# Kernel optimization log

Measured on AMD Instinct MI355X. Metric: run time of the kernel, lower is better.

## Reference

```python
import jax, jax.numpy as jnp
import numpy as np

H = 2  # num_heads hardcoded in the torch module


def setup_inputs() -> dict:
    key = jax.random.key(0)
    ks = jax.random.split(key, 10)
    B, S, D = 8, 2048, 512
    s = 0.02
    return {
        "rgb": jax.random.normal(ks[0], (B, S, D), jnp.float32),
        "event": jax.random.normal(ks[1], (B, S, D), jnp.float32),
        "w_rgb": jax.random.normal(ks[2], (D, D), jnp.float32) * s,
        "b_rgb": jnp.zeros((D,), jnp.float32),
        "w_event": jax.random.normal(ks[3], (D, D), jnp.float32) * s,
        "b_event": jnp.zeros((D,), jnp.float32),
        "w_in": jax.random.normal(ks[4], (3 * D, D), jnp.float32) * s,   # packed QKV in_proj, torch layout
        "b_in": jnp.zeros((3 * D,), jnp.float32),
        "w_out": jax.random.normal(ks[5], (D, D), jnp.float32) * s,
        "b_out": jnp.zeros((D,), jnp.float32),
    }


def _mha(q_in, kv_in, w_in, b_in, w_out, b_out):
    """torch nn.MultiheadAttention with key==value==kv_in, batch-first math."""
    B, S, D = q_in.shape
    hd = D // H
    q = q_in @ w_in[:D].T + b_in[:D]
    k = kv_in @ w_in[D:2 * D].T + b_in[D:2 * D]
    v = kv_in @ w_in[2 * D:].T + b_in[2 * D:]
    q = q.reshape(B, S, H, hd) * (1.0 / np.sqrt(hd))
    k = k.reshape(B, S, H, hd)
    v = v.reshape(B, S, H, hd)
    scores = jnp.einsum('bqhd,bkhd->bhqk', q, k)          # [B,H,S,S]
    attn = jax.nn.softmax(scores, axis=-1)
    out = jnp.einsum('bhqk,bkhd->bqhd', attn, v).reshape(B, S, D)
    return out @ w_out.T + b_out


def reference(rgb, event, w_rgb, b_rgb, w_event, b_event, w_in, b_in, w_out, b_out):
    rgb_p = rgb @ w_rgb.T + b_rgb
    event_p = event @ w_event.T + b_event
    # same attention weights used for both cross directions
    event_attn = _mha(rgb_p, event_p, w_in, b_in, w_out, b_out)
    rgb_attn = _mha(event_p, rgb_p, w_in, b_in, w_out, b_out)
    gate = jax.nn.sigmoid(jnp.sum(rgb_p * event_p, axis=-1, keepdims=True))
    fused = gate * event_attn + (1.0 - gate) * rgb_attn
    return fused + (rgb_p + event_p) * 0.5
```

## Files before the change

kernel.cpp:

```cpp
#include <hip/hip_runtime.h>
#include <hip/hip_bf16.h>
#include <stdint.h>


typedef __bf16 bf16_t;
typedef __bf16 bf16x8 __attribute__((ext_vector_type(8)));
typedef float f32x4 __attribute__((ext_vector_type(4)));
typedef float f32x16 __attribute__((ext_vector_type(16)));
typedef unsigned int u32;

typedef void gvoid_t __attribute__((address_space(1)));
typedef void svoid_t __attribute__((address_space(3)));

__device__ inline void gload16(const void* g, void* l) {
    __builtin_amdgcn_global_load_lds((gvoid_t*)g, (svoid_t*)l, 16, 0, 0);
}

__device__ inline u32 cvtpk_bf16(float lo, float hi) {
    u32 r;
    asm("v_cvt_pk_bf16_f32 %0, %1, %2" : "=v"(r) : "v"(lo), "v"(hi));
    return r;
}

__global__ __launch_bounds__(256) void f2b_kernel(const float* __restrict__ in,
                                                  bf16_t* __restrict__ out, int n8) {
    int i = blockIdx.x * 256 + threadIdx.x;
    if (i >= n8) return;
    const float4* p = reinterpret_cast<const float4*>(in) + (size_t)i * 2;
    float4 a = p[0], b = p[1];
    bf16x8 o;
    o[0] = (bf16_t)a.x; o[1] = (bf16_t)a.y; o[2] = (bf16_t)a.z; o[3] = (bf16_t)a.w;
    o[4] = (bf16_t)b.x; o[5] = (bf16_t)b.y; o[6] = (bf16_t)b.z; o[7] = (bf16_t)b.w;
    reinterpret_cast<bf16x8*>(out)[i] = o;
}

template <int MODE>
__global__ __launch_bounds__(256) void gemm_bt(const bf16_t* __restrict__ A,
                                               const bf16_t* __restrict__ Bw,
                                               const float* __restrict__ bias,
                                               void* __restrict__ Cout,
                                               const bf16_t* __restrict__ r1,
                                               const bf16_t* __restrict__ r2,
                                               bf16_t* __restrict__ qdst,
                                               bf16_t* __restrict__ kdst,
                                               bf16_t* __restrict__ vdst,
                                               int M, int N, int K) {
    __shared__ __align__(16) bf16_t As[128][64];
    __shared__ __align__(16) bf16_t Bs[128][64];
    const int tid = threadIdx.x, lane = tid & 63, w = tid >> 6;
    const int l16 = lane & 15, l4 = lane >> 4;
    const int wm = w >> 1, wn = w & 1;
    const size_t a0 = (size_t)blockIdx.y * 128;
    const size_t b0 = (size_t)blockIdx.x * 128;
    f32x4 acc[4][4] = {};
    const int srow = w * 32 + (lane >> 3);
    const int scol = (lane & 7) * 8;
    for (int kt = 0; kt < K; kt += 64) {
        __syncthreads();
#pragma unroll
        for (int i = 0; i < 4; ++i) {
            gload16(A + (a0 + srow + i * 8) * (size_t)K + kt + scol, &As[w * 32 + i * 8][0]);
            gload16(Bw + (b0 + srow + i * 8) * (size_t)K + kt + scol, &Bs[w * 32 + i * 8][0]);
        }
        __syncthreads();
#pragma unroll
        for (int kk = 0; kk < 2; ++kk) {
            bf16x8 af[4], bfr[4];
#pragma unroll
            for (int mi = 0; mi < 4; ++mi)
                af[mi] = *reinterpret_cast<const bf16x8*>(&As[wm * 64 + mi * 16 + l16][kk * 32 + l4 * 8]);
#pragma unroll
            for (int ni = 0; ni < 4; ++ni)
                bfr[ni] = *reinterpret_cast<const bf16x8*>(&Bs[wn * 64 + ni * 16 + l16][kk * 32 + l4 * 8]);
#pragma unroll
            for (int mi = 0; mi < 4; ++mi)
#pragma unroll
                for (int ni = 0; ni < 4; ++ni)
                    acc[mi][ni] = __builtin_amdgcn_mfma_f32_16x16x32_bf16(af[mi], bfr[ni], acc[mi][ni], 0, 0, 0);
        }
    }
#pragma unroll
    for (int mi = 0; mi < 4; ++mi) {
#pragma unroll
        for (int ni = 0; ni < 4; ++ni) {
            int col = (int)b0 + wn * 64 + ni * 16 + l16;
            float bs = bias[col];
            int row0 = (int)a0 + wm * 64 + mi * 16 + l4 * 4;
            float vv[4];
#pragma unroll
            for (int r = 0; r < 4; ++r) vv[r] = acc[mi][ni][r] + bs;
            if (MODE == 0) {
#pragma unroll
                for (int r = 0; r < 4; ++r)
                    ((bf16_t*)Cout)[(size_t)(row0 + r) * N + col] = (bf16_t)vv[r];
            } else if (MODE == 2) {
#pragma unroll
                for (int r = 0; r < 4; ++r) {
                    size_t idx = (size_t)(row0 + r) * N + col;
                    ((float*)Cout)[idx] = vv[r] + 0.5f * ((float)r1[idx] + (float)r2[idx]);
                }
            } else {
                if (col < 512) {
#pragma unroll
                    for (int r = 0; r < 4; ++r)
                        qdst[(size_t)(row0 + r) * 512 + col] = (bf16_t)(vv[r] * 0.0625f);
                } else if (col < 1024) {
                    int cc = col - 512, h = cc >> 8, d = cc & 255;
#pragma unroll
                    for (int r = 0; r < 4; ++r) {
                        int row = row0 + r;
                        int bh = (row >> 11) * 2 + h, seq = row & 2047;
                        kdst[((size_t)(bh * 64 + (seq >> 5))) * 8192 + (d >> 3) * 256 +
                             (seq & 31) * 8 + (d & 7)] = (bf16_t)vv[r];
                    }
                } else {
                    int cc = col - 1024, h = cc >> 8, d = cc & 255;
                    int bh = (row0 >> 11) * 2 + h, seq = row0 & 2047;
                    size_t idx = ((size_t)(bh * 64 + (seq >> 5))) * 8192 +
                                 ((seq >> 3) & 3) * 2048 + d * 8 + (seq & 7);
                    union { bf16_t h4[4]; uint2 u8; } pk;
#pragma unroll
                    for (int r = 0; r < 4; ++r) pk.h4[r] = (bf16_t)vv[r];
                    *reinterpret_cast<uint2*>(&vdst[idx]) = pk.u8;
                }
            }
        }
    }
}

__global__ __launch_bounds__(256) void gate_kernel(const bf16_t* __restrict__ rp,
                                                   const bf16_t* __restrict__ ep,
                                                   float* __restrict__ gate) {
    int row = blockIdx.x * 4 + (threadIdx.x >> 6);
    int lane = threadIdx.x & 63;
    bf16x8 a = reinterpret_cast<const bf16x8*>(rp + (size_t)row * 512)[lane];
    bf16x8 b = reinterpret_cast<const bf16x8*>(ep + (size_t)row * 512)[lane];
    float s = 0.f;
#pragma unroll
    for (int j = 0; j < 8; ++j) s += (float)a[j] * (float)b[j];
#pragma unroll
    for (int off = 32; off; off >>= 1) s += __shfl_xor(s, off, 64);
    if (lane == 0) gate[row] = 1.f / (1.f + __expf(-s));
}

__global__ __launch_bounds__(256, 2) void attn_kernel(const bf16_t* __restrict__ qbr,
                                                      const bf16_t* __restrict__ qbe,
                                                      const bf16_t* __restrict__ kbr,
                                                      const bf16_t* __restrict__ kbe,
                                                      const bf16_t* __restrict__ vbr,
                                                      const bf16_t* __restrict__ vbe,
                                                      bf16_t* __restrict__ out0,
                                                      bf16_t* __restrict__ out1) {
    __shared__ __align__(16) bf16_t smem[32768];
    const int bid = blockIdx.x;
    const int qb = bid >> 5;
    const int combo = bid & 31;
    const int dir = combo >> 4;
    const int bh = combo & 15;
    const int b = bh >> 1, h = bh & 1;
    const bf16_t* Qb = dir ? qbe : qbr;
    const bf16_t* Kc = dir ? kbr : kbe;
    const bf16_t* Vc = dir ? vbr : vbe;
    bf16_t* osrc = dir ? out1 : out0;
    const int tid = threadIdx.x;
    const int w = tid >> 6, l = tid & 63;
    const int l31 = l & 31, hi = l >> 5;
    const int q0w = qb * 128 + w * 32;

    const bf16_t* qp = Qb + ((size_t)(b * 2048 + q0w + l31)) * 512 + h * 256 + hi * 8;
    bf16x8 qf[16];
#pragma unroll
    for (int dch = 0; dch < 16; ++dch)
        qf[dch] = *reinterpret_cast<const bf16x8*>(qp + dch * 16);

    f32x16 O[8] = {};
    float mrun = -1e30f, lrun = 0.f;

    const bf16_t* kq = Kc + (size_t)bh * 524288 + (w * 2048 + l * 8);
    const bf16_t* vq = Vc + (size_t)bh * 524288 + (w * 2048 + l * 8);

#define STAGE(t, nb)                                              \
    do {                                                          \
        const bf16_t* ks_ = kq + (size_t)(t) * 8192;              \
        const bf16_t* vs_ = vq + (size_t)(t) * 8192;              \
        bf16_t* lk_ = &smem[(nb) * 16384 + w * 2048];             \
        bf16_t* lv_ = &smem[(nb) * 16384 + 8192 + w * 2048];      \
        gload16(ks_, lk_);                                        \
        gload16(ks_ + 512, lk_ + 512);                            \
        gload16(ks_ + 1024, lk_ + 1024);                          \
        gload16(ks_ + 1536, lk_ + 1536);                          \
        gload16(vs_, lv_);                                        \
        gload16(vs_ + 512, lv_ + 512);                            \
        gload16(vs_ + 1024, lv_ + 1024);                          \
        gload16(vs_ + 1536, lv_ + 1536);                          \
    } while (0)

    STAGE(0, 0);

    for (int kt2 = 0; kt2 < 64; ++kt2) {
        asm volatile("s_waitcnt vmcnt(0)" ::: "memory");
        __builtin_amdgcn_s_barrier();
        asm volatile("" ::: "memory");
        if (kt2 < 63) STAGE(kt2 + 1, (kt2 + 1) & 1);
        asm volatile("" ::: "memory");

        const int cb = kt2 & 1;
        const bf16_t* kb = &smem[cb * 16384 + hi * 256 + l31 * 8];
        const bf16_t* vb = &smem[cb * 16384 + 8192 + hi * 2048 + l31 * 8];

        f32x16 st = {};
#pragma unroll
        for (int dch = 0; dch < 16; ++dch) {
            bf16x8 kf = *reinterpret_cast<const bf16x8*>(kb + dch * 512);
            st = __builtin_amdgcn_mfma_f32_32x32x16_bf16(kf, qf[dch], st, 0, 0, 0);
        }

        float mx = -1e30f;
#pragma unroll
        for (int r = 0; r < 16; ++r) mx = fmaxf(mx, st[r]);
        mx = fmaxf(mx, __shfl_xor(mx, 32, 64));
        if (__any(mx - mrun > 8.f)) {
            float mnew = fmaxf(mrun, mx);
            float sc = __expf(mrun - mnew);
            mrun = mnew;
            lrun *= sc;
#pragma unroll
            for (int r = 0; r < 16; ++r) {
                int qr = (r & 3) + 8 * (r >> 2) + 4 * hi;
                float scr = __shfl(sc, qr, 64);
#pragma unroll
                for (int g = 0; g < 8; ++g) O[g][r] *= scr;
            }
        }
        float lsum = 0.f;
        u32 W[8];
#pragma unroll
        for (int m = 0; m < 8; ++m) {
            float plo = __expf(st[2 * m] - mrun);
            float phi_ = __expf(st[2 * m + 1] - mrun);
            lsum += plo + phi_;
            W[m] = cvtpk_bf16(plo, phi_);
        }
        lsum += __shfl_xor(lsum, 32, 64);
        lrun += lsum;

#pragma unroll
        for (int s = 0; s < 2; ++s) {
            u32 t0 = hi ? W[4 * s] : W[4 * s + 2];
            u32 t1 = hi ? W[4 * s + 1] : W[4 * s + 3];
            u32 r0 = (u32)__shfl_xor((int)t0, 32, 64);
            u32 r1 = (u32)__shfl_xor((int)t1, 32, 64);
            union { u32 uw[4]; bf16x8 v; } a;
            a.uw[0] = hi ? r0 : W[4 * s];
            a.uw[1] = hi ? r1 : W[4 * s + 1];
            a.uw[2] = hi ? W[4 * s + 2] : r0;
            a.uw[3] = hi ? W[4 * s + 3] : r1;
#pragma unroll
            for (int g = 0; g < 8; ++g) {
                bf16x8 vf = *reinterpret_cast<const bf16x8*>(vb + s * 4096 + g * 256);
                O[g] = __builtin_amdgcn_mfma_f32_32x32x16_bf16(a.v, vf, O[g], 0, 0, 0);
            }
        }
    }
#undef STAGE

#pragma unroll
    for (int r = 0; r < 16; ++r) {
        int qr = (r & 3) + 8 * (r >> 2) + 4 * hi;
        float linv = 1.0f / __shfl(lrun, qr, 64);
        size_t rowoff = ((size_t)(b * 2048 + q0w + qr)) * 512 + h * 256 + l31;
#pragma unroll
        for (int g = 0; g < 8; ++g)
            osrc[rowoff + g * 32] = (bf16_t)(O[g][r] * linv);
    }
}

__global__ __launch_bounds__(256) void mix_kernel(const bf16_t* __restrict__ a1,
                                                  const bf16_t* __restrict__ a2,
                                                  const float* __restrict__ gate,
                                                  bf16_t* __restrict__ outm) {
    int i = blockIdx.x * 256 + threadIdx.x;
    int m = i >> 6;
    float g = gate[m];
    bf16x8 x = reinterpret_cast<const bf16x8*>(a1)[i];
    bf16x8 y = reinterpret_cast<const bf16x8*>(a2)[i];
    bf16x8 o;
#pragma unroll
    for (int j = 0; j < 8; ++j) o[j] = (bf16_t)(g * (float)x[j] + (1.f - g) * (float)y[j]);
    reinterpret_cast<bf16x8*>(outm)[i] = o;
}

extern "C" void kernel_launch(void* const* d_in, const int* in_sizes, int n_in,
                              void* d_out, int out_size, void* d_ws, size_t ws_size,
                              hipStream_t stream) {
    const float* rgb = (const float*)d_in[0];
    const float* event = (const float*)d_in[1];
    const float* w_rgb = (const float*)d_in[2];
    const float* b_rgb = (const float*)d_in[3];
    const float* w_event = (const float*)d_in[4];
    const float* b_event = (const float*)d_in[5];
    const float* w_in = (const float*)d_in[6];
    const float* b_in = (const float*)d_in[7];
    const float* w_out = (const float*)d_in[8];
    const float* b_out = (const float*)d_in[9];
    float* out = (float*)d_out;

    const int M = 16384;
    const size_t MB16 = (size_t)16 * 1024 * 1024;
    char* ws = (char*)d_ws;
    bf16_t* wrgb_bf = (bf16_t*)(ws + 0);
    bf16_t* wevt_bf = (bf16_t*)(ws + 524288);
    bf16_t* wout_bf = (bf16_t*)(ws + 1048576);
    bf16_t* win_bf = (bf16_t*)(ws + 1572864);
    float* gate = (float*)(ws + 3145728);
    bf16_t* bufA = (bf16_t*)(ws + 4194304);
    bf16_t* bufB = (bf16_t*)(ws + 4194304 + MB16);
    bf16_t* rgbp = (bf16_t*)(ws + 4194304 + 2 * MB16);
    bf16_t* evtp = (bf16_t*)(ws + 4194304 + 3 * MB16);
    bf16_t* qbr  = (bf16_t*)(ws + 4194304 + 4 * MB16);
    bf16_t* qbe  = (bf16_t*)(ws + 4194304 + 5 * MB16);
    bf16_t* kbr  = (bf16_t*)(ws + 4194304 + 6 * MB16);
    bf16_t* kbe  = (bf16_t*)(ws + 4194304 + 7 * MB16);
    bf16_t* vbr  = (bf16_t*)(ws + 4194304 + 8 * MB16);
    bf16_t* vbe  = (bf16_t*)(ws + 4194304 + 9 * MB16);
    bf16_t* mixed = (bf16_t*)(ws + 4194304 + 10 * MB16);

    dim3 blk(256);
    f2b_kernel<<<4096, blk, 0, stream>>>(rgb, bufA, M * 512 / 8);
    f2b_kernel<<<4096, blk, 0, stream>>>(event, bufB, M * 512 / 8);
    f2b_kernel<<<128, blk, 0, stream>>>(w_rgb, wrgb_bf, 512 * 512 / 8);
    f2b_kernel<<<128, blk, 0, stream>>>(w_event, wevt_bf, 512 * 512 / 8);
    f2b_kernel<<<384, blk, 0, stream>>>(w_in, win_bf, 1536 * 512 / 8);
    f2b_kernel<<<128, blk, 0, stream>>>(w_out, wout_bf, 512 * 512 / 8);
    gemm_bt<0><<<dim3(4, 128), blk, 0, stream>>>(bufA, wrgb_bf, b_rgb, rgbp, nullptr, nullptr,
                                                 nullptr, nullptr, nullptr, M, 512, 512);
    gemm_bt<0><<<dim3(4, 128), blk, 0, stream>>>(bufB, wevt_bf, b_event, evtp, nullptr, nullptr,
                                                 nullptr, nullptr, nullptr, M, 512, 512);
    gate_kernel<<<4096, blk, 0, stream>>>(rgbp, evtp, gate);
    gemm_bt<1><<<dim3(12, 128), blk, 0, stream>>>(rgbp, win_bf, b_in, nullptr, nullptr, nullptr,
                                                  qbr, kbr, vbr, M, 1536, 512);
    gemm_bt<1><<<dim3(12, 128), blk, 0, stream>>>(evtp, win_bf, b_in, nullptr, nullptr, nullptr,
                                                  qbe, kbe, vbe, M, 1536, 512);
    attn_kernel<<<512, blk, 0, stream>>>(qbr, qbe, kbr, kbe, vbr, vbe, bufA, bufB);
    mix_kernel<<<4096, blk, 0, stream>>>(bufA, bufB, gate, mixed);
    gemm_bt<2><<<dim3(4, 128), blk, 0, stream>>>(mixed, wout_bf, b_out, out, rgbp, evtp,
                                                 nullptr, nullptr, nullptr, M, 512, 512);
}
```

Baseline: 374.1 us.

## Batch launches, fuse gate-mix into out-proj GEMM, use exp2 softmax with setprio

Merges the six fp32-to-bf16 conversions into one kernel and batches the paired rgb/event projection GEMMs into single launches via a doubled grid. The gate mix is folded into the A-tile load of the output GEMM, so the separate mix kernel and its intermediate buffer go away. In attention it folds log2(e) into the Q scale so softmax can use raw v_exp_f32, adds s_setprio around the MFMA sections, and splits the PV loop. The intent is to cut launch overhead and memory round-trips. The cost is that the out-proj GEMM now loads A through registers instead of direct-to-LDS loads.

```diff
diff --git a/kernel.cpp b/kernel.cpp
--- a/kernel.cpp
+++ b/kernel.cpp
@@ -22,46 +22,94 @@
     return r;
 }
 
-__global__ __launch_bounds__(256) void f2b_kernel(const float* __restrict__ in,
-                                                  bf16_t* __restrict__ out, int n8) {
+__device__ inline float exp2v(float x) {
+    float r;
+    asm("v_exp_f32 %0, %1" : "=v"(r) : "v"(x));
+    return r;
+}
+
+__global__ __launch_bounds__(256) void f2b_all(const float* __restrict__ s0, bf16_t* __restrict__ d0,
+                                               const float* __restrict__ s1, bf16_t* __restrict__ d1,
+                                               const float* __restrict__ s2, bf16_t* __restrict__ d2,
+                                               const float* __restrict__ s3, bf16_t* __restrict__ d3,
+                                               const float* __restrict__ s4, bf16_t* __restrict__ d4,
+                                               const float* __restrict__ s5, bf16_t* __restrict__ d5) {
     int i = blockIdx.x * 256 + threadIdx.x;
-    if (i >= n8) return;
-    const float4* p = reinterpret_cast<const float4*>(in) + (size_t)i * 2;
+    const float* s; bf16_t* d; int off;
+    if (i < 1048576)      { s = s0; d = d0; off = i; }
+    else if (i < 2097152) { s = s1; d = d1; off = i - 1048576; }
+    else if (i < 2129920) { s = s2; d = d2; off = i - 2097152; }
+    else if (i < 2162688) { s = s3; d = d3; off = i - 2129920; }
+    else if (i < 2260992) { s = s4; d = d4; off = i - 2162688; }
+    else                  { s = s5; d = d5; off = i - 2260992; }
+    const float4* p = reinterpret_cast<const float4*>(s) + (size_t)off * 2;
     float4 a = p[0], b = p[1];
     bf16x8 o;
     o[0] = (bf16_t)a.x; o[1] = (bf16_t)a.y; o[2] = (bf16_t)a.z; o[3] = (bf16_t)a.w;
     o[4] = (bf16_t)b.x; o[5] = (bf16_t)b.y; o[6] = (bf16_t)b.z; o[7] = (bf16_t)b.w;
-    reinterpret_cast<bf16x8*>(out)[i] = o;
+    reinterpret_cast<bf16x8*>(d)[off] = o;
 }
 
 template <int MODE>
 __global__ __launch_bounds__(256) void gemm_bt(const bf16_t* __restrict__ A,
+                                               const bf16_t* __restrict__ A2,
                                                const bf16_t* __restrict__ Bw,
+                                               const bf16_t* __restrict__ Bw2,
                                                const float* __restrict__ bias,
+                                               const float* __restrict__ bias2,
                                                void* __restrict__ Cout,
+                                               void* __restrict__ Cout2,
                                                const bf16_t* __restrict__ r1,
                                                const bf16_t* __restrict__ r2,
+                                               const float* __restrict__ gate,
                                                bf16_t* __restrict__ qdst,
                                                bf16_t* __restrict__ kdst,
                                                bf16_t* __restrict__ vdst,
-                                               int M, int N, int K) {
+                                               bf16_t* __restrict__ qdst2,
+                                               bf16_t* __restrict__ kdst2,
+                                               bf16_t* __restrict__ vdst2,
+                                               int N, int K) {
     __shared__ __align__(16) bf16_t As[128][64];
     __shared__ __align__(16) bf16_t Bs[128][64];
     const int tid = threadIdx.x, lane = tid & 63, w = tid >> 6;
     const int l16 = lane & 15, l4 = lane >> 4;
     const int wm = w >> 1, wn = w & 1;
-    const size_t a0 = (size_t)blockIdx.y * 128;
+    const bool sec = (MODE != 2) && (blockIdx.y >= 128);
+    const size_t a0 = (size_t)(blockIdx.y & 127) * 128;
     const size_t b0 = (size_t)blockIdx.x * 128;
+    const bf16_t* Ap = sec ? A2 : A;
+    const bf16_t* Bp = sec ? Bw2 : Bw;
+    const float* bp = sec ? bias2 : bias;
     f32x4 acc[4][4] = {};
     const int srow = w * 32 + (lane >> 3);
     const int scol = (lane & 7) * 8;
+    float g4[4];
+    if (MODE == 2) {
+#pragma unroll
+        for (int i = 0; i < 4; ++i) g4[i] = gate[a0 + srow + i * 8];
+    }
     for (int kt = 0; kt < K; kt += 64) {
         __syncthreads();
-#pragma unroll
-        for (int i = 0; i < 4; ++i) {
-            gload16(A + (a0 + srow + i * 8) * (size_t)K + kt + scol, &As[w * 32 + i * 8][0]);
-            gload16(Bw + (b0 + srow + i * 8) * (size_t)K + kt + scol, &Bs[w * 32 + i * 8][0]);
-        }
+        if (MODE == 2) {
+#pragma unroll
+            for (int i = 0; i < 4; ++i) {
+                size_t ro = (a0 + srow + i * 8) * (size_t)K + kt + scol;
+                bf16x8 x = *reinterpret_cast<const bf16x8*>(A + ro);
+                bf16x8 y = *reinterpret_cast<const bf16x8*>(A2 + ro);
+                bf16x8 o;
+#pragma unroll
+                for (int j = 0; j < 8; ++j)
+                    o[j] = (bf16_t)(g4[i] * (float)x[j] + (1.f - g4[i]) * (float)y[j]);
+                *reinterpret_cast<bf16x8*>(&As[srow + i * 8 - (lane >> 3) + (lane >> 3)][scol]) = o;
+            }
+        } else {
+#pragma unroll
+            for (int i = 0; i < 4; ++i)
+                gload16(Ap + (a0 + srow + i * 8) * (size_t)K + kt + scol, &As[w * 32 + i * 8][0]);
+        }
+#pragma unroll
+        for (int i = 0; i < 4; ++i)
+            gload16(Bp + (b0 + srow + i * 8) * (size_t)K + kt + scol, &Bs[w * 32 + i * 8][0]);
         __syncthreads();
 #pragma unroll
         for (int kk = 0; kk < 2; ++kk) {
@@ -79,20 +127,24 @@
                     acc[mi][ni] = __builtin_amdgcn_mfma_f32_16x16x32_bf16(af[mi], bfr[ni], acc[mi][ni], 0, 0, 0);
         }
     }
+    bf16_t* qd = sec ? qdst2 : qdst;
+    bf16_t* kd = sec ? kdst2 : kdst;
+    bf16_t* vd = sec ? vdst2 : vdst;
 #pragma unroll
     for (int mi = 0; mi < 4; ++mi) {
 #pragma unroll
         for (int ni = 0; ni < 4; ++ni) {
             int col = (int)b0 + wn * 64 + ni * 16 + l16;
-            float bs = bias[col];
+            float bs = bp[col];
             int row0 = (int)a0 + wm * 64 + mi * 16 + l4 * 4;
             float vv[4];
 #pragma unroll
             for (int r = 0; r < 4; ++r) vv[r] = acc[mi][ni][r] + bs;
             if (MODE == 0) {
+                bf16_t* Cp = (bf16_t*)(sec ? Cout2 : Cout);
 #pragma unroll
                 for (int r = 0; r < 4; ++r)
-                    ((bf16_t*)Cout)[(size_t)(row0 + r) * N + col] = (bf16_t)vv[r];
+                    Cp[(size_t)(row0 + r) * N + col] = (bf16_t)vv[r];
             } else if (MODE == 2) {
 #pragma unroll
                 for (int r = 0; r < 4; ++r) {
@@ -103,15 +155,15 @@
                 if (col < 512) {
 #pragma unroll
                     for (int r = 0; r < 4; ++r)
-                        qdst[(size_t)(row0 + r) * 512 + col] = (bf16_t)(vv[r] * 0.0625f);
+                        qd[(size_t)(row0 + r) * 512 + col] = (bf16_t)(vv[r] * 0.090168440f);
                 } else if (col < 1024) {
                     int cc = col - 512, h = cc >> 8, d = cc & 255;
 #pragma unroll
                     for (int r = 0; r < 4; ++r) {
                         int row = row0 + r;
                         int bh = (row >> 11) * 2 + h, seq = row & 2047;
-                        kdst[((size_t)(bh * 64 + (seq >> 5))) * 8192 + (d >> 3) * 256 +
-                             (seq & 31) * 8 + (d & 7)] = (bf16_t)vv[r];
+                        kd[((size_t)(bh * 64 + (seq >> 5))) * 8192 + (d >> 3) * 256 +
+                           (seq & 31) * 8 + (d & 7)] = (bf16_t)vv[r];
                     }
                 } else {
                     int cc = col - 1024, h = cc >> 8, d = cc & 255;
@@ -121,7 +173,7 @@
                     union { bf16_t h4[4]; uint2 u8; } pk;
 #pragma unroll
                     for (int r = 0; r < 4; ++r) pk.h4[r] = (bf16_t)vv[r];
-                    *reinterpret_cast<uint2*>(&vdst[idx]) = pk.u8;
+                    *reinterpret_cast<uint2*>(&vd[idx]) = pk.u8;
                 }
             }
         }
@@ -174,25 +226,23 @@
         qf[dch] = *reinterpret_cast<const bf16x8*>(qp + dch * 16);
 
     f32x16 O[8] = {};
+    f32x16 st;
     float mrun = -1e30f, lrun = 0.f;
+    union PA { u32 uw[4]; bf16x8 v; } pa0, pa1;
 
     const bf16_t* kq = Kc + (size_t)bh * 524288 + (w * 2048 + l * 8);
     const bf16_t* vq = Vc + (size_t)bh * 524288 + (w * 2048 + l * 8);
 
-#define STAGE(t, nb)                                              \
-    do {                                                          \
-        const bf16_t* ks_ = kq + (size_t)(t) * 8192;              \
-        const bf16_t* vs_ = vq + (size_t)(t) * 8192;              \
-        bf16_t* lk_ = &smem[(nb) * 16384 + w * 2048];             \
-        bf16_t* lv_ = &smem[(nb) * 16384 + 8192 + w * 2048];      \
-        gload16(ks_, lk_);                                        \
-        gload16(ks_ + 512, lk_ + 512);                            \
-        gload16(ks_ + 1024, lk_ + 1024);                          \
-        gload16(ks_ + 1536, lk_ + 1536);                          \
-        gload16(vs_, lv_);                                        \
-        gload16(vs_ + 512, lv_ + 512);                            \
-        gload16(vs_ + 1024, lv_ + 1024);                          \
-        gload16(vs_ + 1536, lv_ + 1536);                          \
+#define STAGE(T, P)                                                    \
+    do {                                                               \
+        const bf16_t* ks_ = kq + (size_t)(T) * 8192;                   \
+        const bf16_t* vs_ = vq + (size_t)(T) * 8192;                   \
+        bf16_t* lk_ = &smem[(P) * 8192 + w * 2048];                    \
+        bf16_t* lv_ = &smem[16384 + (P) * 8192 + w * 2048];            \
+        gload16(ks_, lk_); gload16(ks_ + 512, lk_ + 512);              \
+        gload16(ks_ + 1024, lk_ + 1024); gload16(ks_ + 1536, lk_ + 1536); \
+        gload16(vs_, lv_); gload16(vs_ + 512, lv_ + 512);              \
+        gload16(vs_ + 1024, lv_ + 1024); gload16(vs_ + 1536, lv_ + 1536); \
     } while (0)
 
     STAGE(0, 0);
@@ -200,28 +250,29 @@
     for (int kt2 = 0; kt2 < 64; ++kt2) {
         asm volatile("s_waitcnt vmcnt(0)" ::: "memory");
         __builtin_amdgcn_s_barrier();
-        asm volatile("" ::: "memory");
         if (kt2 < 63) STAGE(kt2 + 1, (kt2 + 1) & 1);
-        asm volatile("" ::: "memory");
 
         const int cb = kt2 & 1;
-        const bf16_t* kb = &smem[cb * 16384 + hi * 256 + l31 * 8];
-        const bf16_t* vb = &smem[cb * 16384 + 8192 + hi * 2048 + l31 * 8];
-
-        f32x16 st = {};
+        const bf16_t* kb = &smem[cb * 8192 + hi * 256 + l31 * 8];
+        const bf16_t* vb = &smem[16384 + cb * 8192 + hi * 2048 + l31 * 8];
+
+#pragma unroll
+        for (int r = 0; r < 16; ++r) st[r] = 0.f;
+        __builtin_amdgcn_s_setprio(1);
 #pragma unroll
         for (int dch = 0; dch < 16; ++dch) {
             bf16x8 kf = *reinterpret_cast<const bf16x8*>(kb + dch * 512);
             st = __builtin_amdgcn_mfma_f32_32x32x16_bf16(kf, qf[dch], st, 0, 0, 0);
         }
-
-        float mx = -1e30f;
-#pragma unroll
-        for (int r = 0; r < 16; ++r) mx = fmaxf(mx, st[r]);
+        __builtin_amdgcn_s_setprio(0);
+
+        float mx = st[0];
+#pragma unroll
+        for (int r = 1; r < 16; ++r) mx = fmaxf(mx, st[r]);
         mx = fmaxf(mx, __shfl_xor(mx, 32, 64));
         if (__any(mx - mrun > 8.f)) {
             float mnew = fmaxf(mrun, mx);
-            float sc = __expf(mrun - mnew);
+            float sc = exp2v(mrun - mnew);
             mrun = mnew;
             lrun *= sc;
 #pragma unroll
@@ -236,31 +287,40 @@
         u32 W[8];
 #pragma unroll
         for (int m = 0; m < 8; ++m) {
-            float plo = __expf(st[2 * m] - mrun);
-            float phi_ = __expf(st[2 * m + 1] - mrun);
+            float plo = exp2v(st[2 * m] - mrun);
+            float phi_ = exp2v(st[2 * m + 1] - mrun);
             lsum += plo + phi_;
             W[m] = cvtpk_bf16(plo, phi_);
         }
         lsum += __shfl_xor(lsum, 32, 64);
         lrun += lsum;
-
-#pragma unroll
-        for (int s = 0; s < 2; ++s) {
-            u32 t0 = hi ? W[4 * s] : W[4 * s + 2];
-            u32 t1 = hi ? W[4 * s + 1] : W[4 * s + 3];
+        {
+            u32 t0 = hi ? W[0] : W[2], t1 = hi ? W[1] : W[3];
             u32 r0 = (u32)__shfl_xor((int)t0, 32, 64);
             u32 r1 = (u32)__shfl_xor((int)t1, 32, 64);
-            union { u32 uw[4]; bf16x8 v; } a;
-            a.uw[0] = hi ? r0 : W[4 * s];
-            a.uw[1] = hi ? r1 : W[4 * s + 1];
-            a.uw[2] = hi ? W[4 * s + 2] : r0;
-            a.uw[3] = hi ? W[4 * s + 3] : r1;
-#pragma unroll
-            for (int g = 0; g < 8; ++g) {
-                bf16x8 vf = *reinterpret_cast<const bf16x8*>(vb + s * 4096 + g * 256);
-                O[g] = __builtin_amdgcn_mfma_f32_32x32x16_bf16(a.v, vf, O[g], 0, 0, 0);
-            }
-        }
+            pa0.uw[0] = hi ? r0 : W[0]; pa0.uw[1] = hi ? r1 : W[1];
+            pa0.uw[2] = hi ? W[2] : r0; pa0.uw[3] = hi ? W[3] : r1;
+        }
+        {
+            u32 t0 = hi ? W[4] : W[6], t1 = hi ? W[5] : W[7];
+            u32 r0 = (u32)__shfl_xor((int)t0, 32, 64);
+            u32 r1 = (u32)__shfl_xor((int)t1, 32, 64);
+            pa1.uw[0] = hi ? r0 : W[4]; pa1.uw[1] = hi ? r1 : W[5];
+            pa1.uw[2] = hi ? W[6] : r0; pa1.uw[3] = hi ? W[7] : r1;
+        }
+
+        __builtin_amdgcn_s_setprio(1);
+#pragma unroll
+        for (int g = 0; g < 8; ++g) {
+            bf16x8 v0 = *reinterpret_cast<const bf16x8*>(vb + g * 256);
+            O[g] = __builtin_amdgcn_mfma_f32_32x32x16_bf16(pa0.v, v0, O[g], 0, 0, 0);
+        }
+#pragma unroll
+        for (int g = 0; g < 8; ++g) {
+            bf16x8 v1 = *reinterpret_cast<const bf16x8*>(vb + 4096 + g * 256);
+            O[g] = __builtin_amdgcn_mfma_f32_32x32x16_bf16(pa1.v, v1, O[g], 0, 0, 0);
+        }
+        __builtin_amdgcn_s_setprio(0);
     }
 #undef STAGE
 
@@ -273,21 +333,6 @@
         for (int g = 0; g < 8; ++g)
             osrc[rowoff + g * 32] = (bf16_t)(O[g][r] * linv);
     }
-}
-
-__global__ __launch_bounds__(256) void mix_kernel(const bf16_t* __restrict__ a1,
-                                                  const bf16_t* __restrict__ a2,
-                                                  const float* __restrict__ gate,
-                                                  bf16_t* __restrict__ outm) {
-    int i = blockIdx.x * 256 + threadIdx.x;
-    int m = i >> 6;
-    float g = gate[m];
-    bf16x8 x = reinterpret_cast<const bf16x8*>(a1)[i];
-    bf16x8 y = reinterpret_cast<const bf16x8*>(a2)[i];
-    bf16x8 o;
-#pragma unroll
-    for (int j = 0; j < 8; ++j) o[j] = (bf16_t)(g * (float)x[j] + (1.f - g) * (float)y[j]);
-    reinterpret_cast<bf16x8*>(outm)[i] = o;
 }
 
 extern "C" void kernel_launch(void* const* d_in, const int* in_sizes, int n_in,
@@ -305,7 +350,6 @@
     const float* b_out = (const float*)d_in[9];
     float* out = (float*)d_out;
 
-    const int M = 16384;
     const size_t MB16 = (size_t)16 * 1024 * 1024;
     char* ws = (char*)d_ws;
     bf16_t* wrgb_bf = (bf16_t*)(ws + 0);
@@ -323,26 +367,21 @@
     bf16_t* kbe  = (bf16_t*)(ws + 4194304 + 7 * MB16);
     bf16_t* vbr  = (bf16_t*)(ws + 4194304 + 8 * MB16);
     bf16_t* vbe  = (bf16_t*)(ws + 4194304 + 9 * MB16);
-    bf16_t* mixed = (bf16_t*)(ws + 4194304 + 10 * MB16);
 
     dim3 blk(256);
-    f2b_kernel<<<4096, blk, 0, stream>>>(rgb, bufA, M * 512 / 8);
-    f2b_kernel<<<4096, blk, 0, stream>>>(event, bufB, M * 512 / 8);
-    f2b_kernel<<<128, blk, 0, stream>>>(w_rgb, wrgb_bf, 512 * 512 / 8);
-    f2b_kernel<<<128, blk, 0, stream>>>(w_event, wevt_bf, 512 * 512 / 8);
-    f2b_kernel<<<384, blk, 0, stream>>>(w_in, win_bf, 1536 * 512 / 8);
-    f2b_kernel<<<128, blk, 0, stream>>>(w_out, wout_bf, 512 * 512 / 8);
-    gemm_bt<0><<<dim3(4, 128), blk, 0, stream>>>(bufA, wrgb_bf, b_rgb, rgbp, nullptr, nullptr,
-                                                 nullptr, nullptr, nullptr, M, 512, 512);
-    gemm_bt<0><<<dim3(4, 128), blk, 0, stream>>>(bufB, wevt_bf, b_event, evtp, nullptr, nullptr,
-                                                 nullptr, nullptr, nullptr, M, 512, 512);
+    f2b_all<<<8960, blk, 0, stream>>>(rgb, bufA, event, bufB, w_rgb, wrgb_bf,
+                                      w_event, wevt_bf, w_in, win_bf, w_out, wout_bf);
+    gemm_bt<0><<<dim3(4, 256), blk, 0, stream>>>(bufA, bufB, wrgb_bf, wevt_bf, b_rgb, b_event,
+                                                 rgbp, evtp, nullptr, nullptr, nullptr,
+                                                 nullptr, nullptr, nullptr, nullptr, nullptr,
+                                                 nullptr, 512, 512);
     gate_kernel<<<4096, blk, 0, stream>>>(rgbp, evtp, gate);
-    gemm_bt<1><<<dim3(12, 128), blk, 0, stream>>>(rgbp, win_bf, b_in, nullptr, nullptr, nullptr,
-                                                  qbr, kbr, vbr, M, 1536, 512);
-    gemm_bt<1><<<dim3(12, 128), blk, 0, stream>>>(evtp, win_bf, b_in, nullptr, nullptr, nullptr,
-                                                  qbe, kbe, vbe, M, 1536, 512);
+    gemm_bt<1><<<dim3(12, 256), blk, 0, stream>>>(rgbp, evtp, win_bf, win_bf, b_in, b_in,
+                                                  nullptr, nullptr, nullptr, nullptr, nullptr,
+                                                  qbr, kbr, vbr, qbe, kbe, vbe, 1536, 512);
     attn_kernel<<<512, blk, 0, stream>>>(qbr, qbe, kbr, kbe, vbr, vbe, bufA, bufB);
-    mix_kernel<<<4096, blk, 0, stream>>>(bufA, bufB, gate, mixed);
-    gemm_bt<2><<<dim3(4, 128), blk, 0, stream>>>(mixed, wout_bf, b_out, out, rgbp, evtp,
-                                                 nullptr, nullptr, nullptr, M, 512, 512);
-}
+    gemm_bt<2><<<dim3(4, 128), blk, 0, stream>>>(bufA, bufB, wout_bf, nullptr, b_out, nullptr,
+                                                 out, nullptr, rgbp, evtp, gate,
+                                                 nullptr, nullptr, nullptr, nullptr, nullptr,
+                                                 nullptr, 512, 512);
+}
```

Result: faster. 355.8 us (-4.9%).
